# Kernel optimization log

Hardware: AMD Instinct MI355X
Metric: run time of the kernel (lower is better)

The kernel has to match this reference:

```python
import jax, jax.numpy as jnp
import numpy as np

# Tensor layout: x is [b, c, d, h, w, p, q, r] = [batch, channels, D, H, W, pd, ph, pw]
LETTERS = 'bcdhwpqr'

def axial_linear(x, W, b, axis, S, C):
    """LinearAlongDims1 over dims [1, axis]: jointly mixes channels and one
    spatial/patch axis. Torch flattens in (spatial, channel) order, so the
    (S*C, S*C) weight is reshaped to [S_out, C_out, S_in, C_in]."""
    a = LETTERS[axis]
    W4 = W.reshape(S, C, S, C)
    out_sub = LETTERS.replace('c', 'Y').replace(a, 'X')
    y = jnp.einsum(f'{LETTERS},XY{a}c->{out_sub}', x, W4)
    bshape = [1] * 8
    bshape[1] = C
    bshape[axis] = S
    return y + b.reshape(S, C).T.reshape(bshape)


def _make_linear_params(key, n):
    kw, kb = jax.random.split(key)
    bound = 1.0 / np.sqrt(n)
    W = jax.random.uniform(kw, (n, n), jnp.float32, -bound, bound)
    b = jax.random.uniform(kb, (n,), jnp.float32, -bound, bound)
    return W, b


def setup_inputs() -> dict:
    key = jax.random.key(0)
    ks = jax.random.split(key, 7)
    B, C, D, P = 2, 64, 16, 4
    x = jax.random.normal(ks[0], (B, C, D, D, D, P, P, P), jnp.float32)
    w_d, b_d = _make_linear_params(ks[1], C * D)      # image_d: dims [1,2]
    w_h, b_h = _make_linear_params(ks[2], C * D)      # image_h: dims [1,3]
    w_w, b_w = _make_linear_params(ks[3], C * D)      # image_w: dims [1,4]
    w_pd, b_pd = _make_linear_params(ks[4], C * P)    # patch_d: dims [1,5]
    w_ph, b_ph = _make_linear_params(ks[5], C * P)    # patch_h: dims [1,6]
    w_pw, b_pw = _make_linear_params(ks[6], C * P)    # patch_w: dims [1,7]
    return {
        'x': x,
        'w_d': w_d, 'b_d': b_d, 'w_h': w_h, 'b_h': b_h, 'w_w': w_w, 'b_w': b_w,
        'w_pd': w_pd, 'b_pd': b_pd, 'w_ph': w_ph, 'b_ph': b_ph,
        'w_pw': w_pw, 'b_pw': b_pw,
    }


def reference(x, w_d, b_d, w_h, b_h, w_w, b_w,
              w_pd, b_pd, w_ph, b_ph, w_pw, b_pw):
    C = x.shape[1]
    D = x.shape[2]
    P = x.shape[5]
    y = axial_linear(x, w_pd, b_pd, 5, P, C)
    y = y + axial_linear(x, w_ph, b_ph, 6, P, C)
    y = y + axial_linear(x, w_pw, b_pw, 7, P, C)
    y = y + axial_linear(x, w_d, b_d, 2, D, C)
    y = y + axial_linear(x, w_h, b_h, 3, D, C)
    y = y + axial_linear(x, w_w, b_w, 4, D, C)
    # shapes match -> leaky_relu + residual (module returns y; gn(x) is discarded)
    y = x + jax.nn.leaky_relu(y, negative_slope=0.01)
    return y
```

## Files before the change

### kernel.cpp

```cpp
#include <hip/hip_runtime.h>

typedef __attribute__((ext_vector_type(8))) short short8;
typedef __attribute__((ext_vector_type(4))) float floatx4;


__device__ __forceinline__ unsigned short f2bf(float f){
  unsigned int u = __float_as_uint(f);
  u += 0x7FFFu + ((u >> 16) & 1u);
  return (unsigned short)(u >> 16);
}

template<int AX>
__device__ __forceinline__ int tidx(int m, int a, int c){
  if      (AX==0){ int b=m>>14, t=m&16383;                         return (b<<24)|(c<<18)|(a<<14)|t; }
  else if (AX==1){ int b=m>>14, d=(m>>10)&15, t=m&1023;            return (b<<24)|(c<<18)|(d<<14)|(a<<10)|t; }
  else           { int b=m>>14, d=(m>>10)&15, h=(m>>6)&15, t=m&63; return (b<<24)|(c<<18)|(d<<14)|(h<<10)|(a<<6)|t; }
}

template<int AX>
__device__ __forceinline__ int srcbase(int m){
  if      (AX==0) return ((m>>14)<<24) | (((m>>10)&15)<<16) | (((m>>6)&15)<<12) | ((m&63)<<6);
  else if (AX==1) return ((m>>14)<<24) | (((m>>10)&15)<<20) | (((m>>6)&15)<<12) | ((m&63)<<6);
  else            return ((m>>14)<<24) | (((m>>10)&15)<<20) | (((m>>6)&15)<<16) | ((m&63)<<6);
}

#define ASYNC_CP16(g, l) \
  __builtin_amdgcn_global_load_lds( \
      (const __attribute__((address_space(1))) unsigned int*)(g), \
      (__attribute__((address_space(3))) unsigned int*)(l), 16, 0, 0)

__global__ __launch_bounds__(256) void castw_all(
    const float* __restrict__ wa, const float* __restrict__ wb, const float* __restrict__ wc,
    const float* __restrict__ wd_, const float* __restrict__ we, const float* __restrict__ wf,
    unsigned short* oa, unsigned short* ob, unsigned short* oc,
    unsigned short* od, unsigned short* oe, unsigned short* of_){
  int blk = blockIdx.x;
  const float* src; unsigned short* dst; int idx;
  if (blk < 6144){ int wsel = blk >> 11, loc = blk & 2047;
    src = wsel==0?wa:(wsel==1?wb:wc); dst = wsel==0?oa:(wsel==1?ob:oc);
    idx = loc*256 + threadIdx.x; }
  else { int b2 = blk - 6144, wsel = b2 >> 7, loc = b2 & 127;
    src = wsel==0?wd_:(wsel==1?we:wf); dst = wsel==0?od:(wsel==1?oe:of_);
    idx = loc*256 + threadIdx.x; }
  float2 v = ((const float2*)src)[idx];
  ((unsigned int*)dst)[idx] = (unsigned int)f2bf(v.x) | ((unsigned int)f2bf(v.y) << 16);
}

__global__ __launch_bounds__(256) void transpose_cx(const float* __restrict__ x,
                                                    unsigned short* __restrict__ xt){
  __shared__ float T[64][65];
  int b  = blockIdx.x >> 12;
  int s0 = (blockIdx.x & 4095) * 64;
  int t = threadIdx.x;
  int cr = t >> 4, sq = t & 15;
  #pragma unroll
  for (int it = 0; it < 4; it++){
    int c = it*16 + cr;
    float4 v = *(const float4*)(x + (b<<24) + (c<<18) + s0 + sq*4);
    T[c][sq*4+0]=v.x; T[c][sq*4+1]=v.y; T[c][sq*4+2]=v.z; T[c][sq*4+3]=v.w;
  }
  __syncthreads();
  int sw = t >> 2, cq = t & 3;
  unsigned int pk[8];
  #pragma unroll
  for (int i=0;i<8;i++){
    float f0 = T[cq*16 + 2*i    ][sw];
    float f1 = T[cq*16 + 2*i + 1][sw];
    pk[i] = (unsigned int)f2bf(f0) | ((unsigned int)f2bf(f1) << 16);
  }
  uint4* dst = (uint4*)(xt + (b<<24) + ((s0 + sw)<<6) + cq*16);
  dst[0] = make_uint4(pk[0],pk[1],pk[2],pk[3]);
  dst[1] = make_uint4(pk[4],pk[5],pk[6],pk[7]);
}

template<int AXI, bool FIRST>
__device__ __forceinline__ void patch_axis(const unsigned short* __restrict__ xp,
                                           const unsigned short* __restrict__ W,
                                           float* AccL, int w, int l16, int q8){
  floatx4 acc[4][2];
  #pragma unroll
  for (int nt=0;nt<4;nt++)
    #pragma unroll
    for (int mt=0;mt<2;mt++) acc[nt][mt] = (floatx4){0.f,0.f,0.f,0.f};

  #pragma unroll 2
  for (int kit = 0; kit < 8; kit++){
    int a = kit >> 1;
    int chalf = ((kit & 1) << 5) + q8*8;
    short8 bf[2], af[4];
    int u = (AXI==0) ? (a*16 + l16)
          : (AXI==1) ? ((l16>>2)*16 + a*4 + (l16&3))
                     : ((l16>>2)*16 + (l16&3)*4 + a);
    #pragma unroll
    for (int mt = 0; mt < 2; mt++)
      bf[mt] = *(const short8*)(xp + mt*4096 + u*64 + chalf);
    #pragma unroll
    for (int nt = 0; nt < 4; nt++){
      int n = w*64 + nt*16 + l16;
      af[nt] = *(const short8*)(W + n*256 + kit*32 + q8*8);
    }
    #pragma unroll
    for (int nt=0; nt<4; nt++)
      #pragma unroll
      for (int mt=0; mt<2; mt++)
        acc[nt][mt] = __builtin_amdgcn_mfma_f32_16x16x32_bf16(af[nt], bf[mt], acc[nt][mt], 0,0,0);
  }

  int uo = (AXI==0) ? (w*16 + l16)
         : (AXI==1) ? ((l16>>2)*16 + w*4 + (l16&3))
                    : ((l16>>2)*16 + (l16&3)*4 + w);
  #pragma unroll
  for (int nt=0; nt<4; nt++)
    #pragma unroll
    for (int mt=0; mt<2; mt++){
      float* p = AccL + (mt*64 + uo)*65 + nt*16 + q8*4;
      #pragma unroll
      for (int rg=0; rg<4; rg++){
        if (FIRST) p[rg]  = acc[nt][mt][rg];
        else       p[rg] += acc[nt][mt][rg];
      }
    }
}

__global__ __launch_bounds__(256) void patch_fused(const unsigned short* __restrict__ xt,
    const unsigned short* __restrict__ Wp_, const unsigned short* __restrict__ Wq_,
    const unsigned short* __restrict__ Wr_, float* __restrict__ out){
  __shared__ float AccL[2*64*65];
  int pp = blockIdx.x;
  int b = pp >> 11, dpair = pp & 2047;
  const unsigned short* xp = xt + (b<<24) + dpair*8192;
  int t = threadIdx.x, w = t>>6, lane = t&63, q8 = lane>>4, l16 = lane&15;

  patch_axis<0,true >(xp, Wp_, AccL, w, l16, q8);
  __syncthreads();
  patch_axis<1,false>(xp, Wq_, AccL, w, l16, q8);
  __syncthreads();
  patch_axis<2,false>(xp, Wr_, AccL, w, l16, q8);
  __syncthreads();

  int sbase = dpair*128;
  #pragma unroll
  for (int it = 0; it < 32; it++){
    int lin = it*256 + t;
    int c = lin >> 7, rem = lin & 127, pt = rem >> 6, u = rem & 63;
    out[(b<<24) | (c<<18) | (sbase + pt*64 + u)] = AccL[(pt*64+u)*65 + c];
  }
}

template<int AX>
__global__ __launch_bounds__(256) void gemm_img(const unsigned short* __restrict__ xt,
                                                const unsigned short* __restrict__ Wbf,
                                                float* __restrict__ out){
  constexpr int K  = 1024;
  constexpr int SA = (AX==0)?(1<<20):(AX==1)?(1<<16):(1<<12);
  int mt = blockIdx.x >> 3;
  int nt = blockIdx.x & 7;

  __shared__ unsigned short Xs[128*32];
  __shared__ unsigned short Ws[128*32];

  int t = threadIdx.x, lane = t & 63, wid = t >> 6;
  int wn = (wid & 1) << 6, wm = (wid >> 1) << 6;
  int q = lane >> 4, l16 = lane & 15;

  floatx4 acc[4][4];
  #pragma unroll
  for (int i=0;i<4;i++)
    #pragma unroll
    for (int j=0;j<4;j++) acc[i][j] = (floatx4){0.f,0.f,0.f,0.f};

  const unsigned short* Wp = Wbf + (size_t)nt*128*K;

  int row = t >> 2;
  int jj  = (t & 3) ^ ((t >> 3) & 3);
  int base0 = srcbase<AX>(mt*128 + row);
  int base1 = srcbase<AX>(mt*128 + 64 + row);
  const unsigned short* wg0 = Wp + row*K + jj*8;
  const unsigned short* wg1 = Wp + (row+64)*K + jj*8;
  unsigned short* ldsX0 = Xs + wid*512;
  unsigned short* ldsX1 = Xs + 2048 + wid*512;
  unsigned short* ldsW0 = Ws + wid*512;
  unsigned short* ldsW1 = Ws + 2048 + wid*512;

  int xoff[4], woff[4];
  #pragma unroll
  for (int i=0;i<4;i++){
    int rx = wm + i*16 + l16; xoff[i] = rx*32 + ((q ^ ((rx>>1)&3))<<3);
    int rw = wn + i*16 + l16; woff[i] = rw*32 + ((q ^ ((rw>>1)&3))<<3);
  }

  for (int k0 = 0; k0 < K; k0 += 32){
    int aK = k0 >> 6;
    int cc = (k0 & 63) + jj*8;
    ASYNC_CP16(xt + base0 + aK*SA + cc, ldsX0);
    ASYNC_CP16(xt + base1 + aK*SA + cc, ldsX1);
    ASYNC_CP16(wg0 + k0, ldsW0);
    ASYNC_CP16(wg1 + k0, ldsW1);
    __syncthreads();

    short8 wf[4], xf[4];
    #pragma unroll
    for (int i=0;i<4;i++){
      wf[i] = *(const short8*)&Ws[woff[i]];
      xf[i] = *(const short8*)&Xs[xoff[i]];
    }
    #pragma unroll
    for (int i=0;i<4;i++)
      #pragma unroll
      for (int j=0;j<4;j++)
        acc[i][j] = __builtin_amdgcn_mfma_f32_16x16x32_bf16(wf[i], xf[j], acc[i][j], 0,0,0);
    __syncthreads();
  }

  #pragma unroll
  for (int i=0;i<4;i++){
    #pragma unroll
    for (int j=0;j<4;j++){
      int mg = mt*128 + wm + j*16 + l16;
      #pragma unroll
      for (int rg=0; rg<4; rg++){
        int ng = nt*128 + wn + i*16 + q*4 + rg;
        int idx = tidx<AX>(mg, ng>>6, ng&63);
        out[idx] += acc[i][j][rg];
      }
    }
  }
}

__global__ __launch_bounds__(256) void epilogue_k(const float* __restrict__ x,
                                                  float* __restrict__ out,
                                                  const float* __restrict__ bd,
                                                  const float* __restrict__ bh,
                                                  const float* __restrict__ bw,
                                                  const float* __restrict__ bpd,
                                                  const float* __restrict__ bph,
                                                  const float* __restrict__ bpw){
  int tid = blockIdx.x*256 + threadIdx.x;
  int base = tid * 4;
  int c = (base>>18)&63, d = (base>>14)&15, h = (base>>10)&15;
  int w = (base>>6)&15,  p = (base>>4)&3,  qq = (base>>2)&3;
  float bias0 = bd[d*64+c] + bh[h*64+c] + bw[w*64+c] + bpd[p*64+c] + bph[qq*64+c];
  float4 o  = *(float4*)(out + base);
  float4 xv = *(const float4*)(x + base);
  float y;
  y = o.x + bias0 + bpw[0*64+c]; o.x = xv.x + (y >= 0.f ? y : 0.01f*y);
  y = o.y + bias0 + bpw[1*64+c]; o.y = xv.y + (y >= 0.f ? y : 0.01f*y);
  y = o.z + bias0 + bpw[2*64+c]; o.z = xv.z + (y >= 0.f ? y : 0.01f*y);
  y = o.w + bias0 + bpw[3*64+c]; o.w = xv.w + (y >= 0.f ? y : 0.01f*y);
  *(float4*)(out + base) = o;
}

extern "C" void kernel_launch(void* const* d_in, const int* in_sizes, int n_in,
                              void* d_out, int out_size, void* d_ws, size_t ws_size,
                              hipStream_t stream){
  const float* x = (const float*)d_in[0];
  const float* Wsrc[6] = {(const float*)d_in[1], (const float*)d_in[3], (const float*)d_in[5],
                          (const float*)d_in[7], (const float*)d_in[9], (const float*)d_in[11]};
  const float* Bsrc[6] = {(const float*)d_in[2], (const float*)d_in[4], (const float*)d_in[6],
                          (const float*)d_in[8], (const float*)d_in[10], (const float*)d_in[12]};
  float* out = (float*)d_out;
  char* ws = (char*)d_ws;

  const size_t welems[6] = {1024u*1024u, 1024u*1024u, 1024u*1024u,
                            256u*256u, 256u*256u, 256u*256u};
  size_t wOff[6], o = 0;
  for (int i=0;i<6;i++){ wOff[i] = o; o += welems[i]*2; }
  size_t xtOff = (o + 255) & ~(size_t)255;
  unsigned short* xt = (unsigned short*)(ws + xtOff);
  unsigned short* Wbf[6];
  for (int i=0;i<6;i++) Wbf[i] = (unsigned short*)(ws + wOff[i]);

  castw_all<<<6528,256,0,stream>>>(Wsrc[0],Wsrc[1],Wsrc[2],Wsrc[3],Wsrc[4],Wsrc[5],
                                   Wbf[0],Wbf[1],Wbf[2],Wbf[3],Wbf[4],Wbf[5]);
  transpose_cx<<<8192,256,0,stream>>>(x, xt);

  patch_fused<<<4096,256,0,stream>>>(xt, Wbf[3], Wbf[4], Wbf[5], out);

  gemm_img<0><<<2048,256,0,stream>>>(xt, Wbf[0], out);
  gemm_img<1><<<2048,256,0,stream>>>(xt, Wbf[1], out);
  gemm_img<2><<<2048,256,0,stream>>>(xt, Wbf[2], out);

  epilogue_k<<<32768,256,0,stream>>>(x, out, Bsrc[0], Bsrc[1], Bsrc[2], Bsrc[3], Bsrc[4], Bsrc[5]);
}
```

Before: 952.4 us.

## Fuse bias/leaky-relu epilogue into last image GEMM and stage patch tile in LDS

Removes the separate epilogue kernel. Bias sums are precomputed into small image and patch tables inside the weight-cast kernel, and the bias add, leaky ReLU and residual are applied in the final image-axis GEMM's store loop. This drops one full read/write pass over the output. The patch kernel now loads its x tile once into swizzled LDS with async global-to-LDS copies, instead of reading global memory in each of the three axis passes. The fused epilogue does scattered scalar reads of x, and the transposed-axis store pattern may be poorly coalesced.

```diff
diff --git a/kernel.cpp b/kernel.cpp
--- a/kernel.cpp
+++ b/kernel.cpp
@@ -32,18 +32,32 @@
 __global__ __launch_bounds__(256) void castw_all(
     const float* __restrict__ wa, const float* __restrict__ wb, const float* __restrict__ wc,
     const float* __restrict__ wd_, const float* __restrict__ we, const float* __restrict__ wf,
+    const float* __restrict__ bd_, const float* __restrict__ bh_, const float* __restrict__ bw_,
+    const float* __restrict__ bpd_, const float* __restrict__ bph_, const float* __restrict__ bpw_,
     unsigned short* oa, unsigned short* ob, unsigned short* oc,
-    unsigned short* od, unsigned short* oe, unsigned short* of_){
+    unsigned short* od, unsigned short* oe, unsigned short* of_,
+    float* __restrict__ Bimg, float* __restrict__ Bpat){
   int blk = blockIdx.x;
-  const float* src; unsigned short* dst; int idx;
-  if (blk < 6144){ int wsel = blk >> 11, loc = blk & 2047;
-    src = wsel==0?wa:(wsel==1?wb:wc); dst = wsel==0?oa:(wsel==1?ob:oc);
-    idx = loc*256 + threadIdx.x; }
-  else { int b2 = blk - 6144, wsel = b2 >> 7, loc = b2 & 127;
-    src = wsel==0?wd_:(wsel==1?we:wf); dst = wsel==0?od:(wsel==1?oe:of_);
-    idx = loc*256 + threadIdx.x; }
-  float2 v = ((const float2*)src)[idx];
-  ((unsigned int*)dst)[idx] = (unsigned int)f2bf(v.x) | ((unsigned int)f2bf(v.y) << 16);
+  if (blk < 6528){
+    const float* src; unsigned short* dst; int idx;
+    if (blk < 6144){ int wsel = blk >> 11, loc = blk & 2047;
+      src = wsel==0?wa:(wsel==1?wb:wc); dst = wsel==0?oa:(wsel==1?ob:oc);
+      idx = loc*256 + threadIdx.x; }
+    else { int b2 = blk - 6144, wsel = b2 >> 7, loc = b2 & 127;
+      src = wsel==0?wd_:(wsel==1?we:wf); dst = wsel==0?od:(wsel==1?oe:of_);
+      idx = loc*256 + threadIdx.x; }
+    float2 v = ((const float2*)src)[idx];
+    ((unsigned int*)dst)[idx] = (unsigned int)f2bf(v.x) | ((unsigned int)f2bf(v.y) << 16);
+  } else if (blk < 7552){
+    int idx = (blk - 6528)*256 + threadIdx.x;
+    int c = idx & 63, wv = (idx>>6)&15, hv = (idx>>10)&15, dv = idx>>14;
+    Bimg[idx] = bd_[dv*64+c] + bh_[hv*64+c] + bw_[wv*64+c];
+  } else {
+    int idx = (blk - 7552)*256 + threadIdx.x;
+    int c = idx & 63, tt = idx>>6;
+    int p = tt>>4, q = (tt>>2)&3, r = tt&3;
+    Bpat[idx] = bpd_[p*64+c] + bph_[q*64+c] + bpw_[r*64+c];
+  }
 }
 
 __global__ __launch_bounds__(256) void transpose_cx(const float* __restrict__ x,
@@ -74,7 +88,7 @@
 }
 
 template<int AXI, bool FIRST>
-__device__ __forceinline__ void patch_axis(const unsigned short* __restrict__ xp,
+__device__ __forceinline__ void patch_axis(const unsigned short* Xs,
                                            const unsigned short* __restrict__ W,
                                            float* AccL, int w, int l16, int q8){
   floatx4 acc[4][2];
@@ -86,14 +100,17 @@
   #pragma unroll 2
   for (int kit = 0; kit < 8; kit++){
     int a = kit >> 1;
-    int chalf = ((kit & 1) << 5) + q8*8;
     short8 bf[2], af[4];
     int u = (AXI==0) ? (a*16 + l16)
           : (AXI==1) ? ((l16>>2)*16 + a*4 + (l16&3))
                      : ((l16>>2)*16 + (l16&3)*4 + a);
-    #pragma unroll
-    for (int mt = 0; mt < 2; mt++)
-      bf[mt] = *(const short8*)(xp + mt*4096 + u*64 + chalf);
+    int jg = ((kit & 1) << 2) + q8;
+    #pragma unroll
+    for (int mt = 0; mt < 2; mt++){
+      int r = mt*64 + u;
+      int j = jg ^ ((r ^ (r >> 3)) & 7);
+      bf[mt] = *(const short8*)(Xs + r*64 + j*8);
+    }
     #pragma unroll
     for (int nt = 0; nt < 4; nt++){
       int n = w*64 + nt*16 + l16;
@@ -126,16 +143,26 @@
     const unsigned short* __restrict__ Wp_, const unsigned short* __restrict__ Wq_,
     const unsigned short* __restrict__ Wr_, float* __restrict__ out){
   __shared__ float AccL[2*64*65];
+  __shared__ unsigned short Xs[8192];
   int pp = blockIdx.x;
   int b = pp >> 11, dpair = pp & 2047;
   const unsigned short* xp = xt + (b<<24) + dpair*8192;
   int t = threadIdx.x, w = t>>6, lane = t&63, q8 = lane>>4, l16 = lane&15;
 
-  patch_axis<0,true >(xp, Wp_, AccL, w, l16, q8);
-  __syncthreads();
-  patch_axis<1,false>(xp, Wq_, AccL, w, l16, q8);
-  __syncthreads();
-  patch_axis<2,false>(xp, Wr_, AccL, w, l16, q8);
+  #pragma unroll
+  for (int i = 0; i < 4; i++){
+    int L = i*256 + t;
+    int r = L >> 3, jl = L & 7;
+    int jg = jl ^ ((r ^ (r >> 3)) & 7);
+    ASYNC_CP16(xp + r*64 + jg*8, Xs + i*2048 + w*512);
+  }
+  __syncthreads();
+
+  patch_axis<0,true >(Xs, Wp_, AccL, w, l16, q8);
+  __syncthreads();
+  patch_axis<1,false>(Xs, Wq_, AccL, w, l16, q8);
+  __syncthreads();
+  patch_axis<2,false>(Xs, Wr_, AccL, w, l16, q8);
   __syncthreads();
 
   int sbase = dpair*128;
@@ -147,10 +174,13 @@
   }
 }
 
-template<int AX>
+template<int AX, int EPI>
 __global__ __launch_bounds__(256) void gemm_img(const unsigned short* __restrict__ xt,
                                                 const unsigned short* __restrict__ Wbf,
-                                                float* __restrict__ out){
+                                                float* __restrict__ out,
+                                                const float* __restrict__ x,
+                                                const float* __restrict__ Bimg,
+                                                const float* __restrict__ Bpat){
   constexpr int K  = 1024;
   constexpr int SA = (AX==0)?(1<<20):(AX==1)?(1<<16):(1<<12);
   int mt = blockIdx.x >> 3;
@@ -217,37 +247,31 @@
     #pragma unroll
     for (int j=0;j<4;j++){
       int mg = mt*128 + wm + j*16 + l16;
-      #pragma unroll
-      for (int rg=0; rg<4; rg++){
-        int ng = nt*128 + wn + i*16 + q*4 + rg;
-        int idx = tidx<AX>(mg, ng>>6, ng&63);
-        out[idx] += acc[i][j][rg];
+      if (EPI){
+        int d = (mg>>10)&15, h = (mg>>6)&15, tt = mg&63;
+        int n0 = nt*128 + wn + i*16 + q*4;
+        int a = n0 >> 6, c0 = n0 & 63;
+        float4 bi = *(const float4*)(Bimg + (((d*16 + h)*16 + a)*64 + c0));
+        float4 bp = *(const float4*)(Bpat + (tt*64 + c0));
+        float bs0 = bi.x + bp.x, bs1 = bi.y + bp.y, bs2 = bi.z + bp.z, bs3 = bi.w + bp.w;
+        #pragma unroll
+        for (int rg=0; rg<4; rg++){
+          int ng = n0 + rg;
+          int idx = tidx<AX>(mg, ng>>6, ng&63);
+          float bsum = (rg==0)?bs0:(rg==1)?bs1:(rg==2)?bs2:bs3;
+          float y = out[idx] + acc[i][j][rg] + bsum;
+          out[idx] = x[idx] + (y >= 0.f ? y : 0.01f*y);
+        }
+      } else {
+        #pragma unroll
+        for (int rg=0; rg<4; rg++){
+          int ng = nt*128 + wn + i*16 + q*4 + rg;
+          int idx = tidx<AX>(mg, ng>>6, ng&63);
+          out[idx] += acc[i][j][rg];
+        }
       }
     }
   }
-}
-
-__global__ __launch_bounds__(256) void epilogue_k(const float* __restrict__ x,
-                                                  float* __restrict__ out,
-                                                  const float* __restrict__ bd,
-                                                  const float* __restrict__ bh,
-                                                  const float* __restrict__ bw,
-                                                  const float* __restrict__ bpd,
-                                                  const float* __restrict__ bph,
-                                                  const float* __restrict__ bpw){
-  int tid = blockIdx.x*256 + threadIdx.x;
-  int base = tid * 4;
-  int c = (base>>18)&63, d = (base>>14)&15, h = (base>>10)&15;
-  int w = (base>>6)&15,  p = (base>>4)&3,  qq = (base>>2)&3;
-  float bias0 = bd[d*64+c] + bh[h*64+c] + bw[w*64+c] + bpd[p*64+c] + bph[qq*64+c];
-  float4 o  = *(float4*)(out + base);
-  float4 xv = *(const float4*)(x + base);
-  float y;
-  y = o.x + bias0 + bpw[0*64+c]; o.x = xv.x + (y >= 0.f ? y : 0.01f*y);
-  y = o.y + bias0 + bpw[1*64+c]; o.y = xv.y + (y >= 0.f ? y : 0.01f*y);
-  y = o.z + bias0 + bpw[2*64+c]; o.z = xv.z + (y >= 0.f ? y : 0.01f*y);
-  y = o.w + bias0 + bpw[3*64+c]; o.w = xv.w + (y >= 0.f ? y : 0.01f*y);
-  *(float4*)(out + base) = o;
 }
 
 extern "C" void kernel_launch(void* const* d_in, const int* in_sizes, int n_in,
@@ -266,19 +290,23 @@
   size_t wOff[6], o = 0;
   for (int i=0;i<6;i++){ wOff[i] = o; o += welems[i]*2; }
   size_t xtOff = (o + 255) & ~(size_t)255;
+  size_t bimgOff = xtOff + ((size_t)1u<<25)*2;
+  size_t bpatOff = bimgOff + (size_t)16*16*16*64*4;
   unsigned short* xt = (unsigned short*)(ws + xtOff);
+  float* Bimg = (float*)(ws + bimgOff);
+  float* Bpat = (float*)(ws + bpatOff);
   unsigned short* Wbf[6];
   for (int i=0;i<6;i++) Wbf[i] = (unsigned short*)(ws + wOff[i]);
 
-  castw_all<<<6528,256,0,stream>>>(Wsrc[0],Wsrc[1],Wsrc[2],Wsrc[3],Wsrc[4],Wsrc[5],
-                                   Wbf[0],Wbf[1],Wbf[2],Wbf[3],Wbf[4],Wbf[5]);
+  castw_all<<<7616,256,0,stream>>>(Wsrc[0],Wsrc[1],Wsrc[2],Wsrc[3],Wsrc[4],Wsrc[5],
+                                   Bsrc[0],Bsrc[1],Bsrc[2],Bsrc[3],Bsrc[4],Bsrc[5],
+                                   Wbf[0],Wbf[1],Wbf[2],Wbf[3],Wbf[4],Wbf[5],
+                                   Bimg, Bpat);
   transpose_cx<<<8192,256,0,stream>>>(x, xt);
 
   patch_fused<<<4096,256,0,stream>>>(xt, Wbf[3], Wbf[4], Wbf[5], out);
 
-  gemm_img<0><<<2048,256,0,stream>>>(xt, Wbf[0], out);
-  gemm_img<1><<<2048,256,0,stream>>>(xt, Wbf[1], out);
-  gemm_img<2><<<2048,256,0,stream>>>(xt, Wbf[2], out);
-
-  epilogue_k<<<32768,256,0,stream>>>(x, out, Bsrc[0], Bsrc[1], Bsrc[2], Bsrc[3], Bsrc[4], Bsrc[5]);
-}
+  gemm_img<0,0><<<2048,256,0,stream>>>(xt, Wbf[0], out, nullptr, nullptr, nullptr);
+  gemm_img<1,0><<<2048,256,0,stream>>>(xt, Wbf[1], out, nullptr, nullptr, nullptr);
+  gemm_img<2,1><<<2048,256,0,stream>>>(xt, Wbf[2], out, x, Bimg, Bpat);
+}
```

Result: faster. 881.7 us (-7.4%).
